# Kernel optimization log

Hardware: AMD Instinct MI355X
Metric: run time of the kernel (lower is better)

## Reference

```python
import jax, jax.numpy as jnp
import numpy as np
from math import log, sqrt

B, L, D, H, NL = 2, 2048, 512, 8, 4
HD = D // H
BOUND = 1.0 / sqrt(5.0)  # NormalizationLayer init bound


def setup_inputs() -> dict:
    key = jax.random.key(0)
    ks = jax.random.split(key, 12)
    s = 1.0 / sqrt(D)
    return {
        "base": jax.random.normal(ks[0], (B, L, D), jnp.float32),
        "qkv_w": jax.random.normal(ks[1], (NL, 3 * D, D), jnp.float32) * s,
        "qkv_b": jax.random.normal(ks[2], (NL, 3 * D), jnp.float32) * 0.01,
        "f1_w": jax.random.normal(ks[3], (NL, D, D), jnp.float32) * s,
        "f1_b": jax.random.normal(ks[4], (NL, D), jnp.float32) * 0.01,
        "f2_w": jax.random.normal(ks[5], (NL, D, D), jnp.float32) * s,
        "f2_b": jax.random.normal(ks[6], (NL, D), jnp.float32) * 0.01,
        "n1_scale": jax.random.uniform(ks[7], (NL,), jnp.float32, -BOUND, BOUND),
        "n1_bias": jax.random.uniform(ks[8], (NL,), jnp.float32, -BOUND, BOUND),
        "n2_scale": jax.random.uniform(ks[9], (NL,), jnp.float32, -BOUND, BOUND),
        "n2_bias": jax.random.uniform(ks[10], (NL,), jnp.float32, -BOUND, BOUND),
    }


def _timing_signal(seq_dim, model_dim, seq_start=1):
    # seq_len=None path of timing_signal_1d
    nt = model_dim // 2
    inc = log(10000.0) / max(nt - 1, 1)
    inv = jnp.exp(jnp.arange(nt, dtype=jnp.float32) * (-inc))  # [nt]
    pos = jnp.arange(-seq_start, seq_dim - seq_start, dtype=jnp.float32)[:, None]  # [L,1]
    st = pos * inv[None, :]  # [L, nt]
    return jnp.concatenate([jnp.sin(st), jnp.cos(st)], axis=1)[None]  # [1, L, D]


def _norm(x, scale, bias):
    # mean/std over dims (1,2), scalar affine
    m = jnp.mean(x, axis=(1, 2), keepdims=True)
    sd = jnp.sqrt(jnp.mean((x - m) ** 2, axis=(1, 2), keepdims=True))
    return (x - m) / sd * scale + bias


def reference(base, qkv_w, qkv_b, f1_w, f1_b, f2_w, f2_b,
              n1_scale, n1_bias, n2_scale, n2_bias):
    x = base + _timing_signal(L, D).astype(base.dtype)
    for i in range(NL):
        qkv = x @ qkv_w[i].T + qkv_b[i]  # [B,L,3D]
        q, k, v = jnp.split(qkv, 3, axis=2)
        q = q.reshape(B, L, H, HD)
        k = k.reshape(B, L, H, HD)
        v = v.reshape(B, L, H, HD)
        a = jnp.einsum('blhd,bmhd->bhlm', q, k) / sqrt(HD)  # [B,H,L,L]
        a = jax.nn.softmax(a, axis=-1)
        o = jnp.einsum('bhlm,bmhd->blhd', a, v).reshape(B, L, D)
        h = _norm(o @ f1_w[i].T + f1_b[i] + x, n1_scale[i], n1_bias[i])
        x = _norm(jax.nn.relu(h @ f2_w[i].T + f2_b[i]) + h, n2_scale[i], n2_bias[i])
    return x
```

## Files before the change

### kernel.cpp

```cpp
#include <hip/hip_runtime.h>
#include <hip/hip_bf16.h>

#define DEV __device__ __forceinline__

typedef __attribute__((ext_vector_type(8))) short bf16x8;
typedef __attribute__((ext_vector_type(4))) float f32x4;
typedef __attribute__((ext_vector_type(16))) float f32x16;
typedef __attribute__((ext_vector_type(4))) unsigned short u16x4;
typedef __attribute__((ext_vector_type(8))) unsigned short u16x8;


DEV unsigned short f2bf(float f) {
  union { float f; unsigned u; } v; v.f = f;
  unsigned r = v.u + 0x7FFFu + ((v.u >> 16) & 1u);
  return (unsigned short)(r >> 16);
}

DEV float bf2f(unsigned short u) {
  union { unsigned u; float f; } v; v.u = ((unsigned)u) << 16; return v.f;
}

DEV void gload_lds16(const void* g, void* lds) {
  __builtin_amdgcn_global_load_lds(
      (const __attribute__((address_space(1))) unsigned int*)g,
      (__attribute__((address_space(3))) unsigned int*)lds, 16, 0, 0);
}

DEV int swz128(int r, int cb) { return r * 128 + (cb ^ ((r & 7) << 4)); }

__global__ __launch_bounds__(256) void cvt_kernel(const float* __restrict__ s,
                                                  unsigned short* __restrict__ d, int n4) {
  int i = blockIdx.x * 256 + threadIdx.x;
  if (i >= n4) return;
  float4 v = ((const float4*)s)[i];
  u16x4 r; r[0] = f2bf(v.x); r[1] = f2bf(v.y); r[2] = f2bf(v.z); r[3] = f2bf(v.w);
  ((u16x4*)d)[i] = r;
}

__global__ __launch_bounds__(256) void init_x_kernel(const float* __restrict__ base,
                                                     float* __restrict__ xf,
                                                     unsigned short* __restrict__ xb) {
  int i = blockIdx.x * 256 + threadIdx.x;
  int d = i & 511;
  int l = (i >> 9) & 2047;
  const float NEG_INC = -(float)(9.210340371976184 / 255.0);
  int j = d & 255;
  float w = expf((float)j * NEG_INC);
  float ang = (float)(l - 1) * w;
  float ts = (d < 256) ? sinf(ang) : cosf(ang);
  float v = base[i] + ts;
  xf[i] = v;
  xb[i] = f2bf(v);
}

template<int MODE, int BM, int BN, int WR, int WC>
__global__ __launch_bounds__(WR * WC * 64) void gemm_kernel(
    const unsigned short* __restrict__ A,
    const unsigned short* __restrict__ W,
    const float* __restrict__ bias,
    const float* __restrict__ resid,
    unsigned short* __restrict__ outb,
    unsigned short* __restrict__ vtout,
    float* __restrict__ outf,
    float* __restrict__ partials,
    int N) {
  constexpr int T = WR * WC * 64;
  constexpr int WTM = BM / WR, WTN = BN / WC;
  constexpr int MR = WTM / 16, NR = WTN / 16;
  constexpr int IA = BM * 8 / T, IB = BN * 8 / T;
  __shared__ __align__(16) unsigned short Al[2][BM * 64];
  __shared__ __align__(16) unsigned short Bl[2][BN * 64];
  __shared__ float red[WR * WC * 2];
  const int tid = threadIdx.x;
  const int lane = tid & 63, wid = tid >> 6;
  const int wr = wid / WC, wc = wid % WC;
  const int m0 = blockIdx.y * BM, n0 = blockIdx.x * BN;

  auto stage = [&](int kt, int buf) {
#pragma unroll
    for (int it = 0; it < IA; ++it) {
      int c = it * T + tid;
      int row = c >> 3, sub = c & 7;
      gload_lds16((const char*)A + (m0 + row) * 1024 + kt * 128 + sub * 16,
                  (char*)Al[buf] + (it * T + wid * 64) * 16);
    }
#pragma unroll
    for (int it = 0; it < IB; ++it) {
      int c = it * T + tid;
      int row = c >> 3, sub = c & 7;
      gload_lds16((const char*)W + (n0 + row) * 1024 + kt * 128 + sub * 16,
                  (char*)Bl[buf] + (it * T + wid * 64) * 16);
    }
  };

  f32x4 acc[MR][NR];
#pragma unroll
  for (int m = 0; m < MR; ++m)
#pragma unroll
    for (int n = 0; n < NR; ++n) acc[m][n] = (f32x4){0.f, 0.f, 0.f, 0.f};

  stage(0, 0);
  __syncthreads();
  for (int kt = 0; kt < 8; ++kt) {
    int cur = kt & 1;
    if (kt < 7) stage(kt + 1, cur ^ 1);
#pragma unroll
    for (int ks = 0; ks < 2; ++ks) {
      bf16x8 af[MR], bfr[NR];
#pragma unroll
      for (int m = 0; m < MR; ++m)
        af[m] = *(const bf16x8*)&Al[cur][(wr * WTM + m * 16 + (lane & 15)) * 64 + ks * 32 + (lane >> 4) * 8];
#pragma unroll
      for (int n = 0; n < NR; ++n)
        bfr[n] = *(const bf16x8*)&Bl[cur][(wc * WTN + n * 16 + (lane & 15)) * 64 + ks * 32 + (lane >> 4) * 8];
#pragma unroll
      for (int m = 0; m < MR; ++m)
#pragma unroll
        for (int n = 0; n < NR; ++n)
          acc[m][n] = __builtin_amdgcn_mfma_f32_16x16x32_bf16(af[m], bfr[n], acc[m][n], 0, 0, 0);
    }
    __syncthreads();
  }

  float ps = 0.f, ps2 = 0.f;
#pragma unroll
  for (int m = 0; m < MR; ++m) {
    int row = m0 + wr * WTM + m * 16 + ((lane >> 4) << 2);
#pragma unroll
    for (int n = 0; n < NR; ++n) {
      int col = n0 + wc * WTN + n * 16 + (lane & 15);
      float bv = bias[col];
      if (MODE == 0) {
        u16x4 q4;
#pragma unroll
        for (int j = 0; j < 4; ++j) {
          float v = acc[m][n][j] + bv;
          if (col < 512) v *= 0.180336880f;
          unsigned short bf = f2bf(v);
          q4[j] = bf;
          outb[(row + j) * N + col] = bf;
        }
        if (col >= 1024) {
          int c2 = col - 1024;
          size_t va = ((size_t)((row >> 11) * 8 + (c2 >> 6)) * 64 + (c2 & 63)) * 2048 + (row & 2047);
          *(u16x4*)&vtout[va] = q4;
        }
      } else {
#pragma unroll
        for (int j = 0; j < 4; ++j) {
          float v = acc[m][n][j] + bv;
          if (MODE == 2) v = fmaxf(v, 0.f);
          int idx = (row + j) * N + col;
          v += resid[idx];
          outf[idx] = v;
          ps += v; ps2 += v * v;
        }
      }
    }
  }
  if (MODE != 0) {
#pragma unroll
    for (int s = 1; s < 64; s <<= 1) {
      ps += __shfl_xor(ps, s);
      ps2 += __shfl_xor(ps2, s);
    }
    if (lane == 0) { red[wid * 2] = ps; red[wid * 2 + 1] = ps2; }
    __syncthreads();
    if (tid == 0) {
      float s = 0.f, s2 = 0.f;
#pragma unroll
      for (int w = 0; w < WR * WC; ++w) { s += red[w * 2]; s2 += red[w * 2 + 1]; }
      constexpr int YPB = 2048 / BM;
      int batch = blockIdx.y / YPB;
      int slot = (blockIdx.y % YPB) * gridDim.x + blockIdx.x;
      partials[(batch * 256 + slot) * 2] = s;
      partials[(batch * 256 + slot) * 2 + 1] = s2;
    }
  }
}

__global__ __launch_bounds__(256) void attn_kernel(
    const unsigned short* __restrict__ qkv,
    const unsigned short* __restrict__ vT,
    unsigned short* __restrict__ op0,
    unsigned short* __restrict__ op1,
    float* __restrict__ ssums) {
  __shared__ __align__(16) unsigned short Kl[2][64 * 64];
  __shared__ __align__(16) unsigned short Vl[2][64 * 64];
  const int tid = threadIdx.x;
  const int lane = tid & 63, wid = tid >> 6;
  const int lq = lane & 31;
  const int g = lane >> 5;
  const int l0 = blockIdx.x * 128;
  const int bh = blockIdx.y;
  const int b = bh >> 3, h = bh & 7;
  const int sp = blockIdx.z;
  const int qrow = l0 + wid * 32 + lq;

  const size_t qoff = (size_t)b * 2048 * 1536 + h * 64;
  const size_t koff = qoff + 512;
  const size_t voff = (size_t)(b * 8 + h) * 64 * 2048;

  bf16x8 qf[4];
#pragma unroll
  for (int dm = 0; dm < 4; ++dm)
    qf[dm] = *(const bf16x8*)&qkv[qoff + (size_t)qrow * 1536 + dm * 16 + g * 8];

  auto stageKV = [&](int t, int buf) {
#pragma unroll
    for (int it = 0; it < 2; ++it) {
      int c = it * 256 + tid;
      int row = c >> 3, sub = c & 7;
      int sw = (sub * 16) ^ ((row & 7) << 4);
      gload_lds16((const char*)qkv + (koff + (size_t)(t * 64 + row) * 1536) * 2 + sw,
                  (char*)Kl[buf] + (it * 256 + wid * 64) * 16);
    }
#pragma unroll
    for (int it = 0; it < 2; ++it) {
      int c = it * 256 + tid;
      int row = c >> 3, sub = c & 7;
      int sw = (sub * 16) ^ ((row & 7) << 4);
      gload_lds16((const char*)vT + (voff + (size_t)row * 2048 + t * 64) * 2 + sw,
                  (char*)Vl[buf] + (it * 256 + wid * 64) * 16);
    }
  };

  stageKV(sp * 16, 0);
  __syncthreads();

  float ssum = 0.f;
  f32x16 oacc[2];
#pragma unroll
  for (int dn = 0; dn < 2; ++dn)
#pragma unroll
    for (int i = 0; i < 16; ++i) oacc[dn][i] = 0.f;

  auto pack2 = [&](const float* p, bf16x8& paA, bf16x8& paB) {
    unsigned w[8];
#pragma unroll
    for (int j = 0; j < 8; ++j)
      asm("v_cvt_pk_bf16_f32 %0, %1, %2" : "=v"(w[j]) : "v"(p[2 * j]), "v"(p[2 * j + 1]));
    asm("v_permlane32_swap_b32 %0, %1" : "+v"(w[0]), "+v"(w[2]));
    asm("v_permlane32_swap_b32 %0, %1" : "+v"(w[1]), "+v"(w[3]));
    asm("v_permlane32_swap_b32 %0, %1" : "+v"(w[4]), "+v"(w[6]));
    asm("v_permlane32_swap_b32 %0, %1" : "+v"(w[5]), "+v"(w[7]));
    union { unsigned u[4]; bf16x8 v; } a, c;
    a.u[0] = w[2]; a.u[1] = w[3]; a.u[2] = w[0]; a.u[3] = w[1];
    c.u[0] = w[6]; c.u[1] = w[7]; c.u[2] = w[4]; c.u[3] = w[5];
    paA = a.v; paB = c.v;
  };

  for (int tt = 0; tt < 16; ++tt) {
    int cur = tt & 1;
    if (tt < 15) stageKV(sp * 16 + tt + 1, cur ^ 1);

    f32x16 s0, s1;
#pragma unroll
    for (int i = 0; i < 16; ++i) { s0[i] = 0.f; s1[i] = 0.f; }
#pragma unroll
    for (int dm = 0; dm < 4; ++dm) {
      bf16x8 kf0 = *(const bf16x8*)((const char*)Kl[cur] + swz128(lq, dm * 32 + g * 16));
      bf16x8 kf1 = *(const bf16x8*)((const char*)Kl[cur] + swz128(32 + lq, dm * 32 + g * 16));
      s0 = __builtin_amdgcn_mfma_f32_32x32x16_bf16(kf0, qf[dm], s0, 0, 0, 0);
      s1 = __builtin_amdgcn_mfma_f32_32x32x16_bf16(kf1, qf[dm], s1, 0, 0, 0);
    }

    float p0[16], p1[16];
#pragma unroll
    for (int i = 0; i < 16; ++i) { p0[i] = exp2f(s0[i]); p1[i] = exp2f(s1[i]); }

    float a8[8];
#pragma unroll
    for (int i = 0; i < 8; ++i) a8[i] = (p0[i] + p0[i + 8]) + (p1[i] + p1[i + 8]);
#pragma unroll
    for (int i = 0; i < 4; ++i) a8[i] = a8[i] + a8[i + 4];
    float rs = (a8[0] + a8[1]) + (a8[2] + a8[3]);
    rs += __shfl_xor(rs, 32);
    ssum += rs;

    bf16x8 fr[4];
    pack2(p0, fr[0], fr[1]);
    pack2(p1, fr[2], fr[3]);

#pragma unroll
    for (int dn = 0; dn < 2; ++dn) {
#pragma unroll
      for (int q = 0; q < 4; ++q) {
        bf16x8 vf = *(const bf16x8*)((const char*)Vl[cur] +
                                     swz128(dn * 32 + lq, q * 32 + (g ^ 1) * 16));
        oacc[dn] = __builtin_amdgcn_mfma_f32_32x32x16_bf16(vf, fr[q], oacc[dn], 0, 0, 0);
      }
    }
    __syncthreads();
  }

  unsigned short* op = sp ? op1 : op0;
  size_t obase = (size_t)bh * 131072;
#pragma unroll
  for (int dn = 0; dn < 2; ++dn)
#pragma unroll
    for (int ro = 0; ro < 4; ++ro) {
      int d0 = dn * 32 + ro * 8 + g * 4;
      u16x4 o4;
#pragma unroll
      for (int e = 0; e < 4; ++e) o4[e] = f2bf(oacc[dn][ro * 4 + e]);
      *(u16x4*)&op[obase + (size_t)qrow * 64 + d0] = o4;
    }
  if (lane < 32)
    ssums[(size_t)sp * 32768 + (size_t)bh * 2048 + qrow] = ssum;
}

__global__ __launch_bounds__(256) void attn_combine_kernel(
    const unsigned short* __restrict__ op0,
    const unsigned short* __restrict__ op1,
    const float* __restrict__ ssums,
    unsigned short* __restrict__ o) {
  const int tid = threadIdx.x;
  int row = blockIdx.x * 16 + (tid >> 4);
  int c0 = (tid & 15) * 4;
  float inv = 1.f / (ssums[row] + ssums[32768 + row]);
  u16x4 a0 = *(const u16x4*)&op0[(size_t)row * 64 + c0];
  u16x4 a1 = *(const u16x4*)&op1[(size_t)row * 64 + c0];
  int bh = row >> 11, l = row & 2047;
  int b = bh >> 3, h = bh & 7;
  u16x4 r;
#pragma unroll
  for (int e = 0; e < 4; ++e)
    r[e] = f2bf((bf2f(a0[e]) + bf2f(a1[e])) * inv);
  *(u16x4*)&o[((size_t)(b * 2048 + l)) * 512 + h * 64 + c0] = r;
}

__global__ __launch_bounds__(256) void norm_kernel(
    const float* __restrict__ in,
    const float* __restrict__ partials,
    const float* __restrict__ scale_arr,
    const float* __restrict__ bias_arr,
    int layer,
    float* __restrict__ outf,
    unsigned short* __restrict__ outb,
    float* __restrict__ outf2) {
  int i4 = blockIdx.x * 256 + threadIdx.x;
  size_t i = (size_t)i4 * 4;
  int batch = (int)(i >> 20);
  const float* p = partials + batch * 512;
  int lane = threadIdx.x & 63;
  float s = 0.f, s2 = 0.f;
  for (int k = lane; k < 256; k += 64) { s += p[k * 2]; s2 += p[k * 2 + 1]; }
#pragma unroll
  for (int m = 1; m < 64; m <<= 1) { s += __shfl_xor(s, m); s2 += __shfl_xor(s2, m); }
  const float invn = 1.f / 1048576.f;
  float mean = s * invn;
  float var = s2 * invn - mean * mean;
  float a = scale_arr[layer] / sqrtf(var);
  float bi = bias_arr[layer] - mean * a;
  float4 v = *(const float4*)(in + i);
  float4 r;
  r.x = v.x * a + bi; r.y = v.y * a + bi; r.z = v.z * a + bi; r.w = v.w * a + bi;
  *(float4*)(outf + i) = r;
  u16x4 rb; rb[0] = f2bf(r.x); rb[1] = f2bf(r.y); rb[2] = f2bf(r.z); rb[3] = f2bf(r.w);
  *(u16x4*)(outb + i) = rb;
  if (outf2) *(float4*)(outf2 + i) = r;
}

extern "C" void kernel_launch(void* const* d_in, const int* in_sizes, int n_in,
                              void* d_out, int out_size, void* d_ws, size_t ws_size,
                              hipStream_t stream) {
  (void)in_sizes; (void)n_in; (void)out_size; (void)ws_size;
  const float* base  = (const float*)d_in[0];
  const float* qkv_w = (const float*)d_in[1];
  const float* qkv_b = (const float*)d_in[2];
  const float* f1_w  = (const float*)d_in[3];
  const float* f1_b  = (const float*)d_in[4];
  const float* f2_w  = (const float*)d_in[5];
  const float* f2_b  = (const float*)d_in[6];
  const float* n1s   = (const float*)d_in[7];
  const float* n1b   = (const float*)d_in[8];
  const float* n2s   = (const float*)d_in[9];
  const float* n2b   = (const float*)d_in[10];

  char* ws = (char*)d_ws;
  float*          x_f32  = (float*)(ws + 0);
  unsigned short* x_bf   = (unsigned short*)(ws + (8u << 20));
  unsigned short* qkv_bf = (unsigned short*)(ws + (12u << 20));
  unsigned short* o_bf   = (unsigned short*)(ws + (12u << 20));
  unsigned short* h_bf   = (unsigned short*)(ws + (16u << 20));
  unsigned short* vT     = (unsigned short*)(ws + (28u << 20));
  float*          ssums  = (float*)(ws + (32u << 20));
  float*          t_f32  = (float*)(ws + (28u << 20));
  float*          h_f32  = (float*)(ws + (36u << 20));
  unsigned short* op0    = (unsigned short*)(ws + (36u << 20));
  unsigned short* op1    = (unsigned short*)(ws + (40u << 20));
  unsigned short* wq     = (unsigned short*)(ws + (44u << 20));
  unsigned short* w1     = (unsigned short*)(ws + (50u << 20));
  unsigned short* w2     = (unsigned short*)(ws + (52u << 20));
  float*          parts  = (float*)(ws + (54u << 20));

  cvt_kernel<<<3072, 256, 0, stream>>>(qkv_w, wq, 786432);
  cvt_kernel<<<1024, 256, 0, stream>>>(f1_w, w1, 262144);
  cvt_kernel<<<1024, 256, 0, stream>>>(f2_w, w2, 262144);
  init_x_kernel<<<8192, 256, 0, stream>>>(base, x_f32, x_bf);

  for (int L = 0; L < 4; ++L) {
    gemm_kernel<0, 64, 128, 1, 4><<<dim3(12, 64), 256, 0, stream>>>(
        x_bf, wq + L * 786432, qkv_b + L * 1536, nullptr, qkv_bf, vT, nullptr, nullptr, 1536);
    attn_kernel<<<dim3(16, 16, 2), 256, 0, stream>>>(qkv_bf, vT, op0, op1, ssums);
    attn_combine_kernel<<<2048, 256, 0, stream>>>(op0, op1, ssums, o_bf);
    gemm_kernel<1, 64, 64, 2, 2><<<dim3(8, 64), 256, 0, stream>>>(
        o_bf, w1 + L * 262144, f1_b + L * 512, x_f32, nullptr, nullptr, t_f32, parts, 512);
    norm_kernel<<<2048, 256, 0, stream>>>(t_f32, parts, n1s, n1b, L, h_f32, h_bf, nullptr);
    gemm_kernel<2, 64, 64, 2, 2><<<dim3(8, 64), 256, 0, stream>>>(
        h_bf, w2 + L * 262144, f2_b + L * 512, h_f32, nullptr, nullptr, t_f32, parts, 512);
    norm_kernel<<<2048, 256, 0, stream>>>(t_f32, parts, n2s, n2b, L, x_f32, x_bf,
                                          (L == 3) ? (float*)d_out : nullptr);
  }
}
```

Before: 388.7 us.

## Halve attention and FFN GEMM block sizes, add MFMA priority hints

```diff
diff --git a/kernel.cpp b/kernel.cpp
--- a/kernel.cpp
+++ b/kernel.cpp
@@ -113,11 +113,13 @@
 #pragma unroll
       for (int n = 0; n < NR; ++n)
         bfr[n] = *(const bf16x8*)&Bl[cur][(wc * WTN + n * 16 + (lane & 15)) * 64 + ks * 32 + (lane >> 4) * 8];
+      __builtin_amdgcn_s_setprio(1);
 #pragma unroll
       for (int m = 0; m < MR; ++m)
 #pragma unroll
         for (int n = 0; n < NR; ++n)
           acc[m][n] = __builtin_amdgcn_mfma_f32_16x16x32_bf16(af[m], bfr[n], acc[m][n], 0, 0, 0);
+      __builtin_amdgcn_s_setprio(0);
     }
     __syncthreads();
   }
@@ -171,15 +173,16 @@
 #pragma unroll
       for (int w = 0; w < WR * WC; ++w) { s += red[w * 2]; s2 += red[w * 2 + 1]; }
       constexpr int YPB = 2048 / BM;
+      constexpr int SLOTS = YPB * (512 / BN);
       int batch = blockIdx.y / YPB;
       int slot = (blockIdx.y % YPB) * gridDim.x + blockIdx.x;
-      partials[(batch * 256 + slot) * 2] = s;
-      partials[(batch * 256 + slot) * 2 + 1] = s2;
+      partials[(batch * SLOTS + slot) * 2] = s;
+      partials[(batch * SLOTS + slot) * 2 + 1] = s2;
     }
   }
 }
 
-__global__ __launch_bounds__(256) void attn_kernel(
+__global__ __launch_bounds__(128) void attn_kernel(
     const unsigned short* __restrict__ qkv,
     const unsigned short* __restrict__ vT,
     unsigned short* __restrict__ op0,
@@ -191,7 +194,7 @@
   const int lane = tid & 63, wid = tid >> 6;
   const int lq = lane & 31;
   const int g = lane >> 5;
-  const int l0 = blockIdx.x * 128;
+  const int l0 = blockIdx.x * 64;
   const int bh = blockIdx.y;
   const int b = bh >> 3, h = bh & 7;
   const int sp = blockIdx.z;
@@ -208,20 +211,20 @@
 
   auto stageKV = [&](int t, int buf) {
 #pragma unroll
-    for (int it = 0; it < 2; ++it) {
-      int c = it * 256 + tid;
+    for (int it = 0; it < 4; ++it) {
+      int c = it * 128 + tid;
       int row = c >> 3, sub = c & 7;
       int sw = (sub * 16) ^ ((row & 7) << 4);
       gload_lds16((const char*)qkv + (koff + (size_t)(t * 64 + row) * 1536) * 2 + sw,
-                  (char*)Kl[buf] + (it * 256 + wid * 64) * 16);
-    }
-#pragma unroll
-    for (int it = 0; it < 2; ++it) {
-      int c = it * 256 + tid;
+                  (char*)Kl[buf] + (it * 128 + wid * 64) * 16);
+    }
+#pragma unroll
+    for (int it = 0; it < 4; ++it) {
+      int c = it * 128 + tid;
       int row = c >> 3, sub = c & 7;
       int sw = (sub * 16) ^ ((row & 7) << 4);
       gload_lds16((const char*)vT + (voff + (size_t)row * 2048 + t * 64) * 2 + sw,
-                  (char*)Vl[buf] + (it * 256 + wid * 64) * 16);
+                  (char*)Vl[buf] + (it * 128 + wid * 64) * 16);
     }
   };
 
@@ -261,8 +264,10 @@
     for (int dm = 0; dm < 4; ++dm) {
       bf16x8 kf0 = *(const bf16x8*)((const char*)Kl[cur] + swz128(lq, dm * 32 + g * 16));
       bf16x8 kf1 = *(const bf16x8*)((const char*)Kl[cur] + swz128(32 + lq, dm * 32 + g * 16));
+      __builtin_amdgcn_s_setprio(1);
       s0 = __builtin_amdgcn_mfma_f32_32x32x16_bf16(kf0, qf[dm], s0, 0, 0, 0);
       s1 = __builtin_amdgcn_mfma_f32_32x32x16_bf16(kf1, qf[dm], s1, 0, 0, 0);
+      __builtin_amdgcn_s_setprio(0);
     }
 
     float p0[16], p1[16];
@@ -284,12 +289,16 @@
 
 #pragma unroll
     for (int dn = 0; dn < 2; ++dn) {
-#pragma unroll
-      for (int q = 0; q < 4; ++q) {
-        bf16x8 vf = *(const bf16x8*)((const char*)Vl[cur] +
-                                     swz128(dn * 32 + lq, q * 32 + (g ^ 1) * 16));
-        oacc[dn] = __builtin_amdgcn_mfma_f32_32x32x16_bf16(vf, fr[q], oacc[dn], 0, 0, 0);
-      }
+      bf16x8 vf[4];
+#pragma unroll
+      for (int q = 0; q < 4; ++q)
+        vf[q] = *(const bf16x8*)((const char*)Vl[cur] +
+                                 swz128(dn * 32 + lq, q * 32 + (g ^ 1) * 16));
+      __builtin_amdgcn_s_setprio(1);
+#pragma unroll
+      for (int q = 0; q < 4; ++q)
+        oacc[dn] = __builtin_amdgcn_mfma_f32_32x32x16_bf16(vf[q], fr[q], oacc[dn], 0, 0, 0);
+      __builtin_amdgcn_s_setprio(0);
     }
     __syncthreads();
   }
@@ -333,6 +342,7 @@
 __global__ __launch_bounds__(256) void norm_kernel(
     const float* __restrict__ in,
     const float* __restrict__ partials,
+    int nslots,
     const float* __restrict__ scale_arr,
     const float* __restrict__ bias_arr,
     int layer,
@@ -342,10 +352,10 @@
   int i4 = blockIdx.x * 256 + threadIdx.x;
   size_t i = (size_t)i4 * 4;
   int batch = (int)(i >> 20);
-  const float* p = partials + batch * 512;
+  const float* p = partials + batch * nslots * 2;
   int lane = threadIdx.x & 63;
   float s = 0.f, s2 = 0.f;
-  for (int k = lane; k < 256; k += 64) { s += p[k * 2]; s2 += p[k * 2 + 1]; }
+  for (int k = lane; k < nslots; k += 64) { s += p[k * 2]; s2 += p[k * 2 + 1]; }
 #pragma unroll
   for (int m = 1; m < 64; m <<= 1) { s += __shfl_xor(s, m); s2 += __shfl_xor(s2, m); }
   const float invn = 1.f / 1048576.f;
@@ -403,14 +413,14 @@
   for (int L = 0; L < 4; ++L) {
     gemm_kernel<0, 64, 128, 1, 4><<<dim3(12, 64), 256, 0, stream>>>(
         x_bf, wq + L * 786432, qkv_b + L * 1536, nullptr, qkv_bf, vT, nullptr, nullptr, 1536);
-    attn_kernel<<<dim3(16, 16, 2), 256, 0, stream>>>(qkv_bf, vT, op0, op1, ssums);
+    attn_kernel<<<dim3(32, 16, 2), 128, 0, stream>>>(qkv_bf, vT, op0, op1, ssums);
     attn_combine_kernel<<<2048, 256, 0, stream>>>(op0, op1, ssums, o_bf);
-    gemm_kernel<1, 64, 64, 2, 2><<<dim3(8, 64), 256, 0, stream>>>(
+    gemm_kernel<1, 32, 64, 1, 2><<<dim3(8, 128), 128, 0, stream>>>(
         o_bf, w1 + L * 262144, f1_b + L * 512, x_f32, nullptr, nullptr, t_f32, parts, 512);
-    norm_kernel<<<2048, 256, 0, stream>>>(t_f32, parts, n1s, n1b, L, h_f32, h_bf, nullptr);
-    gemm_kernel<2, 64, 64, 2, 2><<<dim3(8, 64), 256, 0, stream>>>(
+    norm_kernel<<<2048, 256, 0, stream>>>(t_f32, parts, 512, n1s, n1b, L, h_f32, h_bf, nullptr);
+    gemm_kernel<2, 32, 64, 1, 2><<<dim3(8, 128), 128, 0, stream>>>(
         h_bf, w2 + L * 262144, f2_b + L * 512, h_f32, nullptr, nullptr, t_f32, parts, 512);
-    norm_kernel<<<2048, 256, 0, stream>>>(t_f32, parts, n2s, n2b, L, x_f32, x_bf,
+    norm_kernel<<<2048, 256, 0, stream>>>(t_f32, parts, 512, n2s, n2b, L, x_f32, x_bf,
                                           (L == 3) ? (float*)d_out : nullptr);
   }
 }
```

New measurement: 390.9 us. Within noise of the previous version (+0.6%).
